# Performance work log

Measured on AMD Instinct MI355X. Metric: run time of the kernel, lower is better.

The kernel has to match this reference:

```python
import jax, jax.numpy as jnp
import numpy as np

SEQ_LEN = 32768
EMBED = 256
HIDDEN = 512
VOCAB = 6
NUM_OUT = 8


def setup_inputs() -> dict:
    key = jax.random.key(0)
    ks = jax.random.split(key, 8)
    g = lambda k, shp, s: (jax.random.normal(k, shp, dtype=jnp.float32) * s)
    return {
        "sequence": jax.random.randint(ks[0], (SEQ_LEN,), 0, VOCAB),
        "emb": g(ks[1], (VOCAB, EMBED), 1.0),
        "W_ih": g(ks[2], (3 * HIDDEN, EMBED), 0.04),
        "W_hh": g(ks[3], (3 * HIDDEN, HIDDEN), 0.04),
        "b_ih": g(ks[4], (3 * HIDDEN,), 0.04),
        "b_hh": g(ks[5], (3 * HIDDEN,), 0.04),
        "W_out": g(ks[6], (NUM_OUT, HIDDEN), 0.04),
        "b_out": g(ks[7], (NUM_OUT,), 0.04),
    }


def reference(sequence, emb, W_ih, W_hh, b_ih, b_hh, W_out, b_out):
    H = W_hh.shape[1]
    # Embedding lookup: (S, E)
    x = emb[sequence]
    # Precompute input-side gate preactivations for all timesteps: (S, 3H)
    gx = x @ W_ih.T + b_ih

    def step(h, gxt):
        gh = W_hh @ h + b_hh  # (3H,)
        r = jax.nn.sigmoid(gxt[:H] + gh[:H])          # reset gate
        z = jax.nn.sigmoid(gxt[H:2 * H] + gh[H:2 * H])  # update gate
        n = jnp.tanh(gxt[2 * H:] + r * gh[2 * H:])      # new gate
        h_new = (1.0 - z) * n + z * h                    # PyTorch GRU update
        return h_new, None

    h0 = jnp.zeros((H,), dtype=gx.dtype)
    hT, _ = jax.lax.scan(step, h0, gx)
    # Linear head on last timestep output (== last hidden state): (NUM_OUT,)
    return W_out @ hT + b_out
```

## Files before the change

### kernel.cpp

```cpp
#include <hip/hip_runtime.h>

#define S_LEN 32768
#define EMB   256
#define HID   512
#define G3H   1536
#define NWG   8
#define NTHR  512
#define NOUT  8

#define WS_GX    0
#define WS_HBUF  9216

__global__ __launch_bounds__(256) void gru_precompute_kernel(
    const float* __restrict__ emb, const float* __restrict__ W_ih,
    const float* __restrict__ b_ih, float* __restrict__ ws)
{
    int idx = blockIdx.x * 256 + threadIdx.x;
    if (idx < 6 * G3H) {
        int v = idx / G3H, r = idx - v * G3H;
        const float* er = emb + v * EMB;
        const float* wr = W_ih + r * EMB;
        float s = 0.f;
        #pragma unroll 8
        for (int e = 0; e < EMB; ++e) s += er[e] * wr[e];
        ws[WS_GX + idx] = s + b_ih[r];
    }
    if (blockIdx.x == 0) {
        for (int j = threadIdx.x; j < 2048; j += 256)
            __hip_atomic_store((int*)&ws[WS_HBUF + j], 0,
                               __ATOMIC_RELAXED, __HIP_MEMORY_SCOPE_AGENT);
    }
}

__global__ __launch_bounds__(512, 2) void gru_persistent_kernel(
    const int* __restrict__ seq, const float* __restrict__ W_hh,
    const float* __restrict__ b_hh, const float* __restrict__ W_out,
    const float* __restrict__ b_out, float* __restrict__ ws,
    float* __restrict__ out)
{
    __shared__ __align__(16) float h_lds[2][544];
    __shared__ float gx_lds[6 * 3 * 64];
    __shared__ float bhn_lds[64];
    __shared__ unsigned char seq_lds[S_LEN];

    const int g    = blockIdx.x;
    const int tid  = threadIdx.x;
    const int wid  = tid >> 6;
    const int lane = tid & 63;
    const int grp  = lane >> 3;
    const int k    = lane & 7;
    const int il   = wid * 8 + grp;
    const int i    = g * 64 + il;

    unsigned long long* hbuf = (unsigned long long*)(ws + WS_HBUF);

    float4 WR[16], WZ[16], WN[16];
    {
        const float4* pr = (const float4*)(W_hh + (size_t)i * HID + k * 64);
        const float4* pz = (const float4*)(W_hh + (size_t)(HID + i) * HID + k * 64);
        const float4* pn = (const float4*)(W_hh + (size_t)(2 * HID + i) * HID + k * 64);
        #pragma unroll
        for (int c = 0; c < 16; ++c) { WR[c] = pr[c]; WZ[c] = pz[c]; WN[c] = pn[c]; }
    }

    for (int idx = tid; idx < 6 * 3 * 64; idx += NTHR) {
        int v = idx / 192, rem = idx - v * 192, gate = rem >> 6, ii = rem & 63;
        float val = ws[WS_GX + v * G3H + gate * HID + g * 64 + ii];
        if (gate < 2) val += b_hh[gate * HID + g * 64 + ii];
        gx_lds[idx] = val;
    }
    if (tid < 64) bhn_lds[tid] = b_hh[2 * HID + g * 64 + tid];
    for (int p = tid; p < S_LEN; p += NTHR) seq_lds[p] = (unsigned char)seq[p];
    __syncthreads();

    for (int t = 0; t < S_LEN; ++t) {
        const int p = t & 1;
        int v = seq_lds[t];
        float gxr = gx_lds[v * 192 + il];
        float gxz = gx_lds[v * 192 + 64 + il];
        float gxn = gx_lds[v * 192 + 128 + il];

        unsigned long long w;
        do {
            w = __hip_atomic_load(&hbuf[p * HID + tid], __ATOMIC_RELAXED,
                                  __HIP_MEMORY_SCOPE_AGENT);
        } while ((unsigned)(w >> 32) != (unsigned)t);
        h_lds[p][tid + ((tid >> 6) << 2)] = __uint_as_float((unsigned)w);
        __syncthreads();

        float ar = 0.f, az = 0.f, an = 0.f;
        const float4* hp = (const float4*)&h_lds[p][k * 68];
        #pragma unroll
        for (int c = 0; c < 16; ++c) {
            float4 hv = hp[c];
            ar += WR[c].x * hv.x; ar += WR[c].y * hv.y;
            ar += WR[c].z * hv.z; ar += WR[c].w * hv.w;
            az += WZ[c].x * hv.x; az += WZ[c].y * hv.y;
            az += WZ[c].z * hv.z; az += WZ[c].w * hv.w;
            an += WN[c].x * hv.x; an += WN[c].y * hv.y;
            an += WN[c].z * hv.z; an += WN[c].w * hv.w;
        }
        #pragma unroll
        for (int m = 1; m < 8; m <<= 1) {
            ar += __shfl_xor(ar, m, 64);
            az += __shfl_xor(az, m, 64);
            an += __shfl_xor(an, m, 64);
        }

        float r = __fdividef(1.f, 1.f + __expf(-(gxr + ar)));
        float z = __fdividef(1.f, 1.f + __expf(-(gxz + az)));
        float nx = gxn + r * (an + bhn_lds[il]);
        float n = 1.f - __fdividef(2.f, 1.f + __expf(2.f * nx));
        float hold = h_lds[p][g * 68 + il];
        float hn = (1.f - z) * n + z * hold;

        if (k == 0) {
            unsigned long long wout =
                ((unsigned long long)(unsigned)(t + 1) << 32) |
                (unsigned long long)__float_as_uint(hn);
            __hip_atomic_store(&hbuf[(1 - p) * HID + i], wout,
                               __ATOMIC_RELAXED, __HIP_MEMORY_SCOPE_AGENT);
        }
    }

    if (g == 0) {
        unsigned long long w;
        do {
            w = __hip_atomic_load(&hbuf[0 * HID + tid], __ATOMIC_RELAXED,
                                  __HIP_MEMORY_SCOPE_AGENT);
        } while ((unsigned)(w >> 32) != (unsigned)S_LEN);
        h_lds[0][tid + ((tid >> 6) << 2)] = __uint_as_float((unsigned)w);
        __syncthreads();
        float s = 0.f;
        #pragma unroll
        for (int m = 0; m < 8; ++m) {
            int j = lane + 64 * m;
            s += W_out[wid * HID + j] * h_lds[0][lane + 68 * m];
        }
        #pragma unroll
        for (int m = 1; m < 64; m <<= 1) s += __shfl_xor(s, m, 64);
        if (lane == 0) out[wid] = s + b_out[wid];
    }
}

extern "C" void kernel_launch(void* const* d_in, const int* in_sizes, int n_in,
                              void* d_out, int out_size, void* d_ws, size_t ws_size,
                              hipStream_t stream) {
    const int*   seq   = (const int*)d_in[0];
    const float* emb   = (const float*)d_in[1];
    const float* W_ih  = (const float*)d_in[2];
    const float* W_hh  = (const float*)d_in[3];
    const float* b_ih  = (const float*)d_in[4];
    const float* b_hh  = (const float*)d_in[5];
    const float* W_out = (const float*)d_in[6];
    const float* b_out = (const float*)d_in[7];
    float* ws = (float*)d_ws;
    float* out = (float*)d_out;

    gru_precompute_kernel<<<36, 256, 0, stream>>>(emb, W_ih, b_ih, ws);
    gru_persistent_kernel<<<NWG, NTHR, 0, stream>>>(seq, W_hh, b_hh, W_out, b_out,
                                                    ws, out);
}
```

Before: 59.82 ms.

## Spread GRU recurrence over 64 workgroups, one hidden row per wave

Repartitions the persistent recurrent kernel from 8 workgroups of 64 rows each to 64 workgroups of 8 rows each. Each wave now owns one hidden unit, with every lane holding 8 weights per gate. The per-row dot product becomes a full 64-lane shuffle reduction, and the padded LDS layout is dropped. The aim is to cut the per-step serial compute on the latency-bound recurrence. In exchange, many more workgroups poll the shared global h buffer each step, and the reduction has a longer shuffle chain.

```diff
diff --git a/kernel.cpp b/kernel.cpp
--- a/kernel.cpp
+++ b/kernel.cpp
@@ -4,7 +4,7 @@
 #define EMB   256
 #define HID   512
 #define G3H   1536
-#define NWG   8
+#define NWG   64
 #define NTHR  512
 #define NOUT  8
 
@@ -32,114 +32,106 @@
     }
 }
 
-__global__ __launch_bounds__(512, 2) void gru_persistent_kernel(
+__global__ __launch_bounds__(512, 1) void gru_persistent_kernel(
     const int* __restrict__ seq, const float* __restrict__ W_hh,
     const float* __restrict__ b_hh, const float* __restrict__ W_out,
     const float* __restrict__ b_out, float* __restrict__ ws,
     float* __restrict__ out)
 {
-    __shared__ __align__(16) float h_lds[2][544];
-    __shared__ float gx_lds[6 * 3 * 64];
-    __shared__ float bhn_lds[64];
+    const int r   = blockIdx.x;
+    const int tid = threadIdx.x;
+    const int w   = tid >> 6;
+    const int l   = tid & 63;
+    const int row = r * 8 + w;
+
+    __shared__ __align__(16) float h_lds[2][HID];
+    __shared__ float gx_lds[6 * 24];
     __shared__ unsigned char seq_lds[S_LEN];
-
-    const int g    = blockIdx.x;
-    const int tid  = threadIdx.x;
-    const int wid  = tid >> 6;
-    const int lane = tid & 63;
-    const int grp  = lane >> 3;
-    const int k    = lane & 7;
-    const int il   = wid * 8 + grp;
-    const int i    = g * 64 + il;
 
     unsigned long long* hbuf = (unsigned long long*)(ws + WS_HBUF);
 
-    float4 WR[16], WZ[16], WN[16];
-    {
-        const float4* pr = (const float4*)(W_hh + (size_t)i * HID + k * 64);
-        const float4* pz = (const float4*)(W_hh + (size_t)(HID + i) * HID + k * 64);
-        const float4* pn = (const float4*)(W_hh + (size_t)(2 * HID + i) * HID + k * 64);
-        #pragma unroll
-        for (int c = 0; c < 16; ++c) { WR[c] = pr[c]; WZ[c] = pz[c]; WN[c] = pn[c]; }
-    }
+    const float4* W4 = (const float4*)W_hh;
+    const size_t br = (size_t)(0 * HID + row) * 128;
+    const size_t bz = (size_t)(1 * HID + row) * 128;
+    const size_t bn = (size_t)(2 * HID + row) * 128;
+    float4 WR0 = W4[br + l], WR1 = W4[br + 64 + l];
+    float4 WZ0 = W4[bz + l], WZ1 = W4[bz + 64 + l];
+    float4 WN0 = W4[bn + l], WN1 = W4[bn + 64 + l];
+    const float bhn = b_hh[2 * HID + row];
 
-    for (int idx = tid; idx < 6 * 3 * 64; idx += NTHR) {
-        int v = idx / 192, rem = idx - v * 192, gate = rem >> 6, ii = rem & 63;
-        float val = ws[WS_GX + v * G3H + gate * HID + g * 64 + ii];
-        if (gate < 2) val += b_hh[gate * HID + g * 64 + ii];
+    for (int idx = tid; idx < 6 * 24; idx += NTHR) {
+        int v = idx / 24, rem = idx - v * 24, gate = rem >> 3, j = rem & 7;
+        float val = ws[WS_GX + v * G3H + gate * HID + r * 8 + j];
+        if (gate < 2) val += b_hh[gate * HID + r * 8 + j];
         gx_lds[idx] = val;
     }
-    if (tid < 64) bhn_lds[tid] = b_hh[2 * HID + g * 64 + tid];
-    for (int p = tid; p < S_LEN; p += NTHR) seq_lds[p] = (unsigned char)seq[p];
+    for (int q = tid; q < S_LEN; q += NTHR) seq_lds[q] = (unsigned char)seq[q];
     __syncthreads();
 
     for (int t = 0; t < S_LEN; ++t) {
         const int p = t & 1;
         int v = seq_lds[t];
-        float gxr = gx_lds[v * 192 + il];
-        float gxz = gx_lds[v * 192 + 64 + il];
-        float gxn = gx_lds[v * 192 + 128 + il];
+        float gxr = gx_lds[v * 24 + w];
+        float gxz = gx_lds[v * 24 + 8 + w];
+        float gxn = gx_lds[v * 24 + 16 + w];
 
-        unsigned long long w;
+        unsigned long long hw;
         do {
-            w = __hip_atomic_load(&hbuf[p * HID + tid], __ATOMIC_RELAXED,
-                                  __HIP_MEMORY_SCOPE_AGENT);
-        } while ((unsigned)(w >> 32) != (unsigned)t);
-        h_lds[p][tid + ((tid >> 6) << 2)] = __uint_as_float((unsigned)w);
+            hw = __hip_atomic_load(&hbuf[p * HID + tid], __ATOMIC_RELAXED,
+                                   __HIP_MEMORY_SCOPE_AGENT);
+        } while ((unsigned)(hw >> 32) != (unsigned)t);
+        h_lds[p][tid] = __uint_as_float((unsigned)hw);
         __syncthreads();
 
-        float ar = 0.f, az = 0.f, an = 0.f;
-        const float4* hp = (const float4*)&h_lds[p][k * 68];
+        const float4* h4 = (const float4*)&h_lds[p][0];
+        float4 h0 = h4[l], h1 = h4[64 + l];
+        float ar = WR0.x * h0.x + WR0.y * h0.y + WR0.z * h0.z + WR0.w * h0.w
+                 + WR1.x * h1.x + WR1.y * h1.y + WR1.z * h1.z + WR1.w * h1.w;
+        float az = WZ0.x * h0.x + WZ0.y * h0.y + WZ0.z * h0.z + WZ0.w * h0.w
+                 + WZ1.x * h1.x + WZ1.y * h1.y + WZ1.z * h1.z + WZ1.w * h1.w;
+        float an = WN0.x * h0.x + WN0.y * h0.y + WN0.z * h0.z + WN0.w * h0.w
+                 + WN1.x * h1.x + WN1.y * h1.y + WN1.z * h1.z + WN1.w * h1.w;
+
         #pragma unroll
-        for (int c = 0; c < 16; ++c) {
-            float4 hv = hp[c];
-            ar += WR[c].x * hv.x; ar += WR[c].y * hv.y;
-            ar += WR[c].z * hv.z; ar += WR[c].w * hv.w;
-            az += WZ[c].x * hv.x; az += WZ[c].y * hv.y;
-            az += WZ[c].z * hv.z; az += WZ[c].w * hv.w;
-            an += WN[c].x * hv.x; an += WN[c].y * hv.y;
-            an += WN[c].z * hv.z; an += WN[c].w * hv.w;
-        }
-        #pragma unroll
-        for (int m = 1; m < 8; m <<= 1) {
+        for (int m = 1; m < 64; m <<= 1) {
             ar += __shfl_xor(ar, m, 64);
             az += __shfl_xor(az, m, 64);
             an += __shfl_xor(an, m, 64);
         }
 
-        float r = __fdividef(1.f, 1.f + __expf(-(gxr + ar)));
-        float z = __fdividef(1.f, 1.f + __expf(-(gxz + az)));
-        float nx = gxn + r * (an + bhn_lds[il]);
-        float n = 1.f - __fdividef(2.f, 1.f + __expf(2.f * nx));
-        float hold = h_lds[p][g * 68 + il];
-        float hn = (1.f - z) * n + z * hold;
+        float rg = __fdividef(1.f, 1.f + __expf(-(gxr + ar)));
+        float zg = __fdividef(1.f, 1.f + __expf(-(gxz + az)));
+        float nx = gxn + rg * (an + bhn);
+        float ng = 1.f - __fdividef(2.f, 1.f + __expf(2.f * nx));
+        float hold = h_lds[p][row];
+        float hn = (1.f - zg) * ng + zg * hold;
 
-        if (k == 0) {
-            unsigned long long wout =
+        if (l == 0) {
+            unsigned long long wo =
                 ((unsigned long long)(unsigned)(t + 1) << 32) |
                 (unsigned long long)__float_as_uint(hn);
-            __hip_atomic_store(&hbuf[(1 - p) * HID + i], wout,
+            __hip_atomic_store(&hbuf[(1 - p) * HID + row], wo,
                                __ATOMIC_RELAXED, __HIP_MEMORY_SCOPE_AGENT);
         }
     }
 
-    if (g == 0) {
-        unsigned long long w;
+    if (r == 0) {
+        unsigned long long hw;
         do {
-            w = __hip_atomic_load(&hbuf[0 * HID + tid], __ATOMIC_RELAXED,
-                                  __HIP_MEMORY_SCOPE_AGENT);
-        } while ((unsigned)(w >> 32) != (unsigned)S_LEN);
-        h_lds[0][tid + ((tid >> 6) << 2)] = __uint_as_float((unsigned)w);
+            hw = __hip_atomic_load(&hbuf[0 * HID + tid], __ATOMIC_RELAXED,
+                                   __HIP_MEMORY_SCOPE_AGENT);
+        } while ((unsigned)(hw >> 32) != (unsigned)S_LEN);
+        h_lds[0][tid] = __uint_as_float((unsigned)hw);
         __syncthreads();
         float s = 0.f;
         #pragma unroll
         for (int m = 0; m < 8; ++m) {
-            int j = lane + 64 * m;
-            s += W_out[wid * HID + j] * h_lds[0][lane + 68 * m];
+            int j = l + 64 * m;
+            s += W_out[w * HID + j] * h_lds[0][j];
         }
         #pragma unroll
         for (int m = 1; m < 64; m <<= 1) s += __shfl_xor(s, m, 64);
-        if (lane == 0) out[wid] = s + b_out[wid];
+        if (l == 0) out[w] = s + b_out[w];
     }
 }
 
```

Result: slower. 88.24 ms (+47.5%).
